# Kernel tuning notes

Measured on AMD Instinct MI355X. Metric: run time of the kernel, lower is better.

## Reference

```python
import jax, jax.numpy as jnp
import numpy as np

TOTAL_WORDS = 10000
EMBED_LEN = 100
SEQ_LEN = 80
BATCH = 2048
UNITS = 1024


def setup_inputs() -> dict:
    key = jax.random.key(0)
    ks = jax.random.split(key, 8)
    inputs = jax.random.randint(ks[0], (BATCH, SEQ_LEN), 0, TOTAL_WORDS)
    s = 0.02
    emb = jax.random.normal(ks[1], (TOTAL_WORDS, EMBED_LEN), jnp.float32) * s
    W0 = jax.random.normal(ks[2], (EMBED_LEN, 4 * UNITS), jnp.float32) * s
    U0 = jax.random.normal(ks[3], (UNITS, 4 * UNITS), jnp.float32) * s
    b0 = jnp.zeros((4 * UNITS,), jnp.float32)
    W1 = jax.random.normal(ks[4], (UNITS, 4 * UNITS), jnp.float32) * s
    U1 = jax.random.normal(ks[5], (UNITS, 4 * UNITS), jnp.float32) * s
    b1 = jnp.zeros((4 * UNITS,), jnp.float32)
    fcW = jax.random.normal(ks[6], (UNITS, 1), jnp.float32) * s
    fcb = jnp.zeros((1,), jnp.float32)
    return {"inputs": inputs, "emb": emb, "W0": W0, "U0": U0, "b0": b0,
            "W1": W1, "U1": U1, "b1": b1, "fcW": fcW, "fcb": fcb}


def _lstm_step(x, h, c, W, U, b):
    # Keras LSTMCell gate order: i, f, g(candidate), o
    z = x @ W + h @ U + b  # [B, 4*units]
    i, f, g, o = jnp.split(z, 4, axis=-1)
    i = jax.nn.sigmoid(i)
    f = jax.nn.sigmoid(f)
    g = jnp.tanh(g)
    o = jax.nn.sigmoid(o)
    c_new = f * c + i * g
    h_new = o * jnp.tanh(c_new)
    return h_new, c_new


def reference(inputs, emb, W0, U0, b0, W1, U1, b1, fcW, fcb):
    x = emb[inputs]                      # [B, T, E]
    xs = jnp.transpose(x, (1, 0, 2))     # [T, B, E] for scan over time
    B = inputs.shape[0]
    U = U0.shape[0]
    init = (jnp.zeros((B, U), x.dtype), jnp.zeros((B, U), x.dtype),
            jnp.zeros((B, U), x.dtype), jnp.zeros((B, U), x.dtype))

    def step(carry, xt):
        h0, c0, h1, c1 = carry
        h0, c0 = _lstm_step(xt, h0, c0, W0, U0, b0)
        h1, c1 = _lstm_step(h0, h1, c1, W1, U1, b1)
        return (h0, c0, h1, c1), None

    (h0, c0, h1, c1), _ = jax.lax.scan(step, init, xs)
    logits = h1 @ fcW + fcb              # [B, 1]
    return jax.nn.sigmoid(logits)
```

## Files before the change

kernel.cpp:

```cpp
#include <hip/hip_runtime.h>

#define DEVI __device__ __forceinline__

typedef __attribute__((ext_vector_type(4))) float f4;
typedef long long i64t;
typedef __attribute__((ext_vector_type(2))) long long i64x2;

DEVI unsigned char f2fp8(float x) {
  int p = __builtin_amdgcn_cvt_pk_fp8_f32(x, x, 0, false);
  return (unsigned char)(p & 0xff);
}
DEVI float fp82f(unsigned char b) {
  return __builtin_amdgcn_cvt_f32_fp8((int)b, 0);
}
DEVI float sigmoidf_(float x) { return 1.f / (1.f + __expf(-x)); }
DEVI float tanhf_(float x) {
  float ax = fabsf(x);
  float e = __expf(-2.f * ax);
  float t = (1.f - e) / (1.f + e);
  return x < 0.f ? -t : t;
}

#define GLDS16(g, l) __builtin_amdgcn_global_load_lds( \
    (const __attribute__((address_space(1))) void*)(g), \
    (__attribute__((address_space(3))) void*)(l), 16, 0, 0)

#define SCALE_UP 64.0f
#define SCALE_DN (1.0f / 4096.0f)

DEVI int mapcol(int k, int r) {
  int c2 = ((k >> 3) & 3) ^ ((r >> 1) & 3);
  return (k & ~63) | (c2 << 4) | (((k >> 5) & 1) << 3) | (k & 7);
}


__global__ void k_conv_emb(const float* __restrict__ emb, unsigned char* __restrict__ ep) {
  int i = blockIdx.x * 256 + threadIdx.x;
  if (i >= 10000 * 128) return;
  int r = i >> 7, c = i & 127;
  ep[r * 128 + mapcol(c, 0)] =
      (c < 100) ? f2fp8(emb[r * 100 + c] * SCALE_UP) : (unsigned char)0;
}

DEVI int permn(int n) {
  int g = n >> 10, u = n & 1023;
  return (u >> 5) * 128 + ((u >> 4) & 1) * 64 + g * 16 + (u & 15);
}

__global__ void k_conv_w0(const float* __restrict__ W0, const float* __restrict__ U0,
                          unsigned char* __restrict__ WT) {
  int i = blockIdx.x * 256 + threadIdx.x;
  if (i >= 4096 * 1152) return;
  int n = i / 1152, k = i - n * 1152;
  float v;
  if (k < 100) v = W0[k * 4096 + n];
  else if (k < 128) v = 0.f;
  else v = U0[(k - 128) * 4096 + n];
  int np = permn(n);
  WT[(size_t)np * 1152 + mapcol(k, np)] = f2fp8(v * SCALE_UP);
}

__global__ void k_conv_w1(const float* __restrict__ W1, const float* __restrict__ U1,
                          unsigned char* __restrict__ WT) {
  int i = blockIdx.x * 256 + threadIdx.x;
  if (i >= 4096 * 2048) return;
  int n = i >> 11, k = i & 2047;
  float v = (k < 1024) ? W1[k * 4096 + n] : U1[(k - 1024) * 4096 + n];
  int np = permn(n);
  WT[(size_t)np * 2048 + mapcol(k, np)] = f2fp8(v * SCALE_UP);
}


template<int K1, int KTOT, bool GATHER>
DEVI void lstm_body(int blk, char* smem,
    const unsigned char* __restrict__ src1,
    const unsigned char* __restrict__ src2,
    const int* __restrict__ idx, int t,
    const unsigned char* __restrict__ WT,
    const float* __restrict__ bias,
    float* __restrict__ cbuf,
    unsigned char* __restrict__ hout)
{
  const int tid = threadIdx.x;
  const int bn = blk & 31;
  const int bm = blk >> 5;
  const int m0 = bm * 128;
  const int n0 = bn * 128;

  const int lr = tid >> 2;
  const int c16 = (tid & 3) * 16;
  const int csw = ((tid & 3) ^ ((tid >> 3) & 3)) * 16;

  const unsigned char* g1[2];
  if (GATHER) {
#pragma unroll
    for (int p = 0; p < 2; ++p) {
      int w = idx[(m0 + p * 64 + lr) * 80 + t];
      g1[p] = src1 + (size_t)w * K1 + csw;
    }
  }

  char* const LA0 = smem;
  char* const LB0 = smem + 8192;
  char* const LA1 = smem + 16384;
  char* const LB1 = smem + 24576;

  auto stage = [&](int kb) {
    char* la = (kb & 1) ? LA1 : LA0;
    char* lb = (kb & 1) ? LB1 : LB0;
    const int kc = kb * 64;
    if (GATHER && kc < K1) {
#pragma unroll
      for (int p = 0; p < 2; ++p)
        GLDS16(g1[p] + kc, la + p * 4096 + tid * 16);
    } else {
#pragma unroll
      for (int p = 0; p < 2; ++p) {
        size_t row = (size_t)(m0 + p * 64 + lr);
        const unsigned char* g = (kc < K1)
            ? (src1 + row * 1024 + kc + c16)
            : (src2 + row * 1024 + (kc - K1) + c16);
        GLDS16(g, la + p * 4096 + tid * 16);
      }
    }
#pragma unroll
    for (int p = 0; p < 2; ++p)
      GLDS16(WT + (size_t)(n0 + p * 64 + lr) * KTOT + kc + c16,
             lb + p * 4096 + tid * 16);
  };

  const int lane = tid & 63;
  const int wv = tid >> 6;
  const int wm = wv >> 1;
  const int wn = wv & 1;
  const int cl = lane & 15;
  const int qd = lane >> 4;
  const int fcl = (cl >> 1) & 3;
  const int aoff = (wm * 64 + cl) * 64 + ((qd ^ fcl) << 4);
  const int boff = (wn * 64 + cl) * 64 + ((qd ^ fcl) << 4);

  f4 acc[4][4];
  const f4 fz = {0.f, 0.f, 0.f, 0.f};
#pragma unroll
  for (int a = 0; a < 4; ++a)
#pragma unroll
    for (int b = 0; b < 4; ++b) acc[a][b] = fz;

  stage(0);

  constexpr int NKB = KTOT / 64;
#pragma unroll 1
  for (int kb = 0; kb < NKB; ++kb) {
    __syncthreads();
    if (kb + 1 < NKB) stage(kb + 1);
    char* la = (kb & 1) ? LA1 : LA0;
    char* lb = (kb & 1) ? LB1 : LB0;
    i64x2 av[4], bv[4];
#pragma unroll
    for (int mi = 0; mi < 4; ++mi)
      av[mi] = *(const i64x2*)(la + aoff + mi * 1024);
#pragma unroll
    for (int j = 0; j < 4; ++j)
      bv[j] = *(const i64x2*)(lb + boff + j * 1024);
#pragma unroll
    for (int mi = 0; mi < 4; ++mi)
#pragma unroll
      for (int j = 0; j < 4; ++j)
        acc[mi][j] = __builtin_amdgcn_mfma_f32_16x16x32_fp8_fp8(
            av[mi][0], bv[j][0], acc[mi][j], 0, 0, 0);
#pragma unroll
    for (int mi = 0; mi < 4; ++mi)
#pragma unroll
      for (int j = 0; j < 4; ++j)
        acc[mi][j] = __builtin_amdgcn_mfma_f32_16x16x32_fp8_fp8(
            av[mi][1], bv[j][1], acc[mi][j], 0, 0, 0);
  }

  const int u = bn * 32 + wn * 16 + cl;
  const int hbase = (u & ~63) | (((u >> 5) & 1) << 3) | (u & 7);
  const int c1u = (u >> 3) & 3;
  const float bi = bias[u];
  const float bff = bias[1024 + u];
  const float bg = bias[2048 + u];
  const float bo = bias[3072 + u];
#pragma unroll
  for (int mi = 0; mi < 4; ++mi) {
    int mbase = m0 + wm * 64 + mi * 16 + qd * 4;
#pragma unroll
    for (int r = 0; r < 4; ++r) {
      int m = mbase + r;
      float gi = sigmoidf_(acc[mi][0][r] * SCALE_DN + bi);
      float gf = sigmoidf_(acc[mi][1][r] * SCALE_DN + bff);
      float gg = tanhf_(acc[mi][2][r] * SCALE_DN + bg);
      float go = sigmoidf_(acc[mi][3][r] * SCALE_DN + bo);
      size_t coff = (size_t)m * 1024 + u;
      float cn = gf * cbuf[coff] + gi * gg;
      cbuf[coff] = cn;
      int c2 = c1u ^ ((qd * 2 + (r >> 1)) & 3);
      hout[(size_t)m * 1024 + (hbase | (c2 << 4))] =
          f2fp8(go * tanhf_(cn) * SCALE_UP);
    }
  }
}

__global__ __launch_bounds__(256, 4) void k_step(
    int mode,
    const unsigned char* embp, const unsigned char* h0in,
    const int* idx, int t,
    const unsigned char* WT0, const float* b0, float* c0, unsigned char* h0out,
    const unsigned char* h0prev, const unsigned char* h1in,
    const unsigned char* WT1, const float* b1, float* c1, unsigned char* h1out)
{
  extern __shared__ char smem[];
  const int blk = blockIdx.x;
  const int tile = (mode == 1) ? (blk >> 1) : blk;
  const bool isL0 = (mode == 0) || (mode == 1 && (blk & 1));
  if (isL0)
    lstm_body<128, 1152, true>(tile, smem, embp, h0in, idx, t,
                               WT0, b0, c0, h0out);
  else
    lstm_body<1024, 2048, false>(tile, smem, h0prev, h1in, nullptr, 0,
                                 WT1, b1, c1, h1out);
}


__global__ void k_fc(const unsigned char* __restrict__ h1,
                     const float* __restrict__ fcW, const float* __restrict__ fcb,
                     float* __restrict__ out) {
  int wv = threadIdx.x >> 6;
  int lane = threadIdx.x & 63;
  int row = blockIdx.x * 4 + wv;
  if (row >= 2048) return;
  const unsigned char* hr = h1 + (size_t)row * 1024;
  float s = 0.f;
  for (int k = lane; k < 1024; k += 64)
    s += fp82f(hr[mapcol(k, row)]) * fcW[k];
#pragma unroll
  for (int off = 32; off > 0; off >>= 1) s += __shfl_down(s, off);
  if (lane == 0) out[row] = sigmoidf_(s * (1.0f / SCALE_UP) + fcb[0]);
}


extern "C" void kernel_launch(void* const* d_in, const int* in_sizes, int n_in,
                              void* d_out, int out_size, void* d_ws, size_t ws_size,
                              hipStream_t stream) {
  const int*   idx = (const int*)d_in[0];
  const float* emb = (const float*)d_in[1];
  const float* W0  = (const float*)d_in[2];
  const float* U0  = (const float*)d_in[3];
  const float* b0  = (const float*)d_in[4];
  const float* W1  = (const float*)d_in[5];
  const float* U1  = (const float*)d_in[6];
  const float* b1  = (const float*)d_in[7];
  const float* fcW = (const float*)d_in[8];
  const float* fcb = (const float*)d_in[9];
  float* out = (float*)d_out;

  char* ws = (char*)d_ws;
  unsigned char* embp = (unsigned char*)(ws);
  unsigned char* WT0  = (unsigned char*)(ws + 1280000);
  unsigned char* WT1  = (unsigned char*)(ws + 5998592);
  unsigned char* h0b[2] = {(unsigned char*)(ws + 14387200),
                           (unsigned char*)(ws + 16484352)};
  unsigned char* h1b[2] = {(unsigned char*)(ws + 18581504),
                           (unsigned char*)(ws + 20678656)};
  float* c0 = (float*)(ws + 22775808);
  float* c1 = (float*)(ws + 31164416);

  hipMemsetAsync(ws + 14387200, 0, 25165824, stream);

  k_conv_emb<<<5000, 256, 0, stream>>>(emb, embp);
  k_conv_w0<<<18432, 256, 0, stream>>>(W0, U0, WT0);
  k_conv_w1<<<32768, 256, 0, stream>>>(W1, U1, WT1);

  k_step<<<512, 256, 32768, stream>>>(0, embp, h0b[1], idx, 0,
                                      WT0, b0, c0, h0b[0],
                                      nullptr, nullptr, WT1, b1, c1, nullptr);
  for (int t = 1; t < 80; ++t) {
    k_step<<<1024, 256, 32768, stream>>>(1, embp, h0b[(t + 1) & 1], idx, t,
                                         WT0, b0, c0, h0b[t & 1],
                                         h0b[(t - 1) & 1], h1b[t & 1],
                                         WT1, b1, c1, h1b[(t + 1) & 1]);
  }
  k_step<<<512, 256, 32768, stream>>>(2, nullptr, nullptr, nullptr, 0,
                                      WT0, b0, c0, nullptr,
                                      h0b[1], h1b[0], WT1, b1, c1, h1b[1]);

  k_fc<<<512, 256, 0, stream>>>(h1b[1], fcW, fcb, out);
}
```

Baseline: 4.316 ms.

## Prefetch B tiles two stages ahead and register-prefetch B fragments

Splits the LDS staging into separate A and B loaders, so B (weight) tiles are issued two k-blocks ahead while A tiles stay one ahead. B fragments for the next k-block are read from LDS into registers during the current iteration, hiding LDS read latency behind the MFMAs. It also interleaves the two k-halves of each MFMA on the same accumulator, which creates back-to-back dependent MFMAs and may add stalls. Register pressure rises from the extra fragment buffer, and compiler-inserted waits on the asynchronous LDS loads may limit the real depth of the prefetch.

```diff
diff --git a/kernel.cpp b/kernel.cpp
--- a/kernel.cpp
+++ b/kernel.cpp
@@ -100,14 +100,11 @@
     }
   }
 
-  char* const LA0 = smem;
-  char* const LB0 = smem + 8192;
-  char* const LA1 = smem + 16384;
-  char* const LB1 = smem + 24576;
-
-  auto stage = [&](int kb) {
-    char* la = (kb & 1) ? LA1 : LA0;
-    char* lb = (kb & 1) ? LB1 : LB0;
+  char* const sA[2] = {smem, smem + 8192};
+  char* const sB[2] = {smem + 16384, smem + 24576};
+
+  auto stageA = [&](int kb) {
+    char* la = sA[kb & 1];
     const int kc = kb * 64;
     if (GATHER && kc < K1) {
 #pragma unroll
@@ -123,6 +120,10 @@
         GLDS16(g, la + p * 4096 + tid * 16);
       }
     }
+  };
+  auto stageB = [&](int kb) {
+    char* lb = sB[kb & 1];
+    const int kc = kb * 64;
 #pragma unroll
     for (int p = 0; p < 2; ++p)
       GLDS16(WT + (size_t)(n0 + p * 64 + lr) * KTOT + kc + c16,
@@ -146,34 +147,46 @@
 #pragma unroll
     for (int b = 0; b < 4; ++b) acc[a][b] = fz;
 
-  stage(0);
-
   constexpr int NKB = KTOT / 64;
+
+  stageA(0);
+  stageB(0);
+  stageB(1);
+  __syncthreads();
+
+  i64x2 av[4], bv[4], bvn[4];
+#pragma unroll
+  for (int j = 0; j < 4; ++j)
+    bv[j] = *(const i64x2*)(sB[0] + boff + j * 1024);
+
 #pragma unroll 1
   for (int kb = 0; kb < NKB; ++kb) {
     __syncthreads();
-    if (kb + 1 < NKB) stage(kb + 1);
-    char* la = (kb & 1) ? LA1 : LA0;
-    char* lb = (kb & 1) ? LB1 : LB0;
-    i64x2 av[4], bv[4];
+    char* la = sA[kb & 1];
 #pragma unroll
     for (int mi = 0; mi < 4; ++mi)
       av[mi] = *(const i64x2*)(la + aoff + mi * 1024);
-#pragma unroll
-    for (int j = 0; j < 4; ++j)
-      bv[j] = *(const i64x2*)(lb + boff + j * 1024);
+    if (kb + 1 < NKB) {
+      char* lbn = sB[(kb + 1) & 1];
+#pragma unroll
+      for (int j = 0; j < 4; ++j)
+        bvn[j] = *(const i64x2*)(lbn + boff + j * 1024);
+      stageA(kb + 1);
+    }
+    if (kb + 2 < NKB) stageB(kb + 2);
 #pragma unroll
     for (int mi = 0; mi < 4; ++mi)
 #pragma unroll
-      for (int j = 0; j < 4; ++j)
+      for (int j = 0; j < 4; ++j) {
         acc[mi][j] = __builtin_amdgcn_mfma_f32_16x16x32_fp8_fp8(
             av[mi][0], bv[j][0], acc[mi][j], 0, 0, 0);
-#pragma unroll
-    for (int mi = 0; mi < 4; ++mi)
-#pragma unroll
-      for (int j = 0; j < 4; ++j)
         acc[mi][j] = __builtin_amdgcn_mfma_f32_16x16x32_fp8_fp8(
             av[mi][1], bv[j][1], acc[mi][j], 0, 0, 0);
+      }
+    if (kb + 1 < NKB) {
+#pragma unroll
+      for (int j = 0; j < 4; ++j) bv[j] = bvn[j];
+    }
   }
 
   const int u = bn * 32 + wn * 16 + cl;
```

Result: slower. 8.618 ms (+99.7%).

## Switch to 16x16x128 scaled FP8 MFMA with 128-wide K tiles

Applied to the files above, without the earlier changes.

Replaces the pair of 16x16x32 FP8 MFMA calls per K=64 chunk with a single gfx950 scaled MFMA over K=128, using unit scales. The K tile doubles to 128, so LDS staging grows to 64 KB, the swizzle changes to an 8-chunk XOR pattern in the weight, embedding and hidden-state layouts, and launch bounds drop to 2 blocks per CU. The aim is fewer MFMA issues, fewer barrier iterations and higher matrix throughput, at the cost of lower occupancy and a larger shared-memory footprint.

```diff
diff --git a/kernel.cpp b/kernel.cpp
--- a/kernel.cpp
+++ b/kernel.cpp
@@ -3,8 +3,8 @@
 #define DEVI __device__ __forceinline__
 
 typedef __attribute__((ext_vector_type(4))) float f4;
-typedef long long i64t;
-typedef __attribute__((ext_vector_type(2))) long long i64x2;
+typedef __attribute__((ext_vector_type(4))) int i32x4;
+typedef __attribute__((ext_vector_type(8))) int i32x8;
 
 DEVI unsigned char f2fp8(float x) {
   int p = __builtin_amdgcn_cvt_pk_fp8_f32(x, x, 0, false);
@@ -27,10 +27,10 @@
 
 #define SCALE_UP 64.0f
 #define SCALE_DN (1.0f / 4096.0f)
+#define SONE 0x7f7f7f7f
 
 DEVI int mapcol(int k, int r) {
-  int c2 = ((k >> 3) & 3) ^ ((r >> 1) & 3);
-  return (k & ~63) | (c2 << 4) | (((k >> 5) & 1) << 3) | (k & 7);
+  return (k & ~127) | (((((k >> 4) & 7) ^ (r & 7))) << 4) | (k & 15);
 }
 
 
@@ -38,8 +38,7 @@
   int i = blockIdx.x * 256 + threadIdx.x;
   if (i >= 10000 * 128) return;
   int r = i >> 7, c = i & 127;
-  ep[r * 128 + mapcol(c, 0)] =
-      (c < 100) ? f2fp8(emb[r * 100 + c] * SCALE_UP) : (unsigned char)0;
+  ep[i] = (c < 100) ? f2fp8(emb[r * 100 + c] * SCALE_UP) : (unsigned char)0;
 }
 
 DEVI int permn(int n) {
@@ -87,36 +86,34 @@
   const int m0 = bm * 128;
   const int n0 = bn * 128;
 
-  const int lr = tid >> 2;
-  const int c16 = (tid & 3) * 16;
-  const int csw = ((tid & 3) ^ ((tid >> 3) & 3)) * 16;
-
-  const unsigned char* g1[2];
+  const int lr = tid >> 3;
+  const int c16 = (tid & 7) * 16;
+  const int csw = ((tid & 7) ^ (lr & 7)) * 16;
+
+  const unsigned char* g1[4];
   if (GATHER) {
 #pragma unroll
-    for (int p = 0; p < 2; ++p) {
-      int w = idx[(m0 + p * 64 + lr) * 80 + t];
+    for (int p = 0; p < 4; ++p) {
+      int w = idx[(m0 + p * 32 + lr) * 80 + t];
       g1[p] = src1 + (size_t)w * K1 + csw;
     }
   }
 
-  char* const LA0 = smem;
-  char* const LB0 = smem + 8192;
-  char* const LA1 = smem + 16384;
-  char* const LB1 = smem + 24576;
+  char* const sA[2] = {smem, smem + 16384};
+  char* const sB[2] = {smem + 32768, smem + 49152};
 
   auto stage = [&](int kb) {
-    char* la = (kb & 1) ? LA1 : LA0;
-    char* lb = (kb & 1) ? LB1 : LB0;
-    const int kc = kb * 64;
+    char* la = sA[kb & 1];
+    char* lb = sB[kb & 1];
+    const int kc = kb * 128;
     if (GATHER && kc < K1) {
 #pragma unroll
-      for (int p = 0; p < 2; ++p)
-        GLDS16(g1[p] + kc, la + p * 4096 + tid * 16);
+      for (int p = 0; p < 4; ++p)
+        GLDS16(g1[p], la + p * 4096 + tid * 16);
     } else {
 #pragma unroll
-      for (int p = 0; p < 2; ++p) {
-        size_t row = (size_t)(m0 + p * 64 + lr);
+      for (int p = 0; p < 4; ++p) {
+        size_t row = (size_t)(m0 + p * 32 + lr);
         const unsigned char* g = (kc < K1)
             ? (src1 + row * 1024 + kc + c16)
             : (src2 + row * 1024 + (kc - K1) + c16);
@@ -124,8 +121,8 @@
       }
     }
 #pragma unroll
-    for (int p = 0; p < 2; ++p)
-      GLDS16(WT + (size_t)(n0 + p * 64 + lr) * KTOT + kc + c16,
+    for (int p = 0; p < 4; ++p)
+      GLDS16(WT + (size_t)(n0 + p * 32 + lr) * KTOT + kc + c16,
              lb + p * 4096 + tid * 16);
   };
 
@@ -135,9 +132,10 @@
   const int wn = wv & 1;
   const int cl = lane & 15;
   const int qd = lane >> 4;
-  const int fcl = (cl >> 1) & 3;
-  const int aoff = (wm * 64 + cl) * 64 + ((qd ^ fcl) << 4);
-  const int boff = (wn * 64 + cl) * 64 + ((qd ^ fcl) << 4);
+  const int ch0 = ((2 * qd) ^ (cl & 7)) << 4;
+  const int ch1 = ((2 * qd + 1) ^ (cl & 7)) << 4;
+  const int abase = (wm * 64 + cl) * 128;
+  const int bbase = (wn * 64 + cl) * 128;
 
   f4 acc[4][4];
   const f4 fz = {0.f, 0.f, 0.f, 0.f};
@@ -148,37 +146,37 @@
 
   stage(0);
 
-  constexpr int NKB = KTOT / 64;
+  constexpr int NKB = KTOT / 128;
 #pragma unroll 1
   for (int kb = 0; kb < NKB; ++kb) {
     __syncthreads();
     if (kb + 1 < NKB) stage(kb + 1);
-    char* la = (kb & 1) ? LA1 : LA0;
-    char* lb = (kb & 1) ? LB1 : LB0;
-    i64x2 av[4], bv[4];
+    char* la = sA[kb & 1];
+    char* lb = sB[kb & 1];
+    i32x8 av[4], bv[4];
+#pragma unroll
+    for (int mi = 0; mi < 4; ++mi) {
+      i32x4 lo = *(const i32x4*)(la + abase + mi * 2048 + ch0);
+      i32x4 hi = *(const i32x4*)(la + abase + mi * 2048 + ch1);
+      av[mi] = __builtin_shufflevector(lo, hi, 0, 1, 2, 3, 4, 5, 6, 7);
+    }
+#pragma unroll
+    for (int j = 0; j < 4; ++j) {
+      i32x4 lo = *(const i32x4*)(lb + bbase + j * 2048 + ch0);
+      i32x4 hi = *(const i32x4*)(lb + bbase + j * 2048 + ch1);
+      bv[j] = __builtin_shufflevector(lo, hi, 0, 1, 2, 3, 4, 5, 6, 7);
+    }
 #pragma unroll
     for (int mi = 0; mi < 4; ++mi)
-      av[mi] = *(const i64x2*)(la + aoff + mi * 1024);
-#pragma unroll
-    for (int j = 0; j < 4; ++j)
-      bv[j] = *(const i64x2*)(lb + boff + j * 1024);
-#pragma unroll
-    for (int mi = 0; mi < 4; ++mi)
 #pragma unroll
       for (int j = 0; j < 4; ++j)
-        acc[mi][j] = __builtin_amdgcn_mfma_f32_16x16x32_fp8_fp8(
-            av[mi][0], bv[j][0], acc[mi][j], 0, 0, 0);
-#pragma unroll
-    for (int mi = 0; mi < 4; ++mi)
-#pragma unroll
-      for (int j = 0; j < 4; ++j)
-        acc[mi][j] = __builtin_amdgcn_mfma_f32_16x16x32_fp8_fp8(
-            av[mi][1], bv[j][1], acc[mi][j], 0, 0, 0);
+        acc[mi][j] = __builtin_amdgcn_mfma_scale_f32_16x16x128_f8f6f4(
+            av[mi], bv[j], acc[mi][j], 0, 0, 0, SONE, 0, SONE);
   }
 
   const int u = bn * 32 + wn * 16 + cl;
-  const int hbase = (u & ~63) | (((u >> 5) & 1) << 3) | (u & 7);
-  const int c1u = (u >> 3) & 3;
+  const int hbase = (u & ~127) | (u & 15);
+  const int c1u = (u >> 4) & 7;
   const float bi = bias[u];
   const float bff = bias[1024 + u];
   const float bg = bias[2048 + u];
@@ -196,14 +194,14 @@
       size_t coff = (size_t)m * 1024 + u;
       float cn = gf * cbuf[coff] + gi * gg;
       cbuf[coff] = cn;
-      int c2 = c1u ^ ((qd * 2 + (r >> 1)) & 3);
+      int c2 = c1u ^ ((qd & 1) * 4 + r);
       hout[(size_t)m * 1024 + (hbase | (c2 << 4))] =
           f2fp8(go * tanhf_(cn) * SCALE_UP);
     }
   }
 }
 
-__global__ __launch_bounds__(256, 4) void k_step(
+__global__ __launch_bounds__(256, 2) void k_step(
     int mode,
     const unsigned char* embp, const unsigned char* h0in,
     const int* idx, int t,
@@ -273,16 +271,16 @@
   k_conv_w0<<<18432, 256, 0, stream>>>(W0, U0, WT0);
   k_conv_w1<<<32768, 256, 0, stream>>>(W1, U1, WT1);
 
-  k_step<<<512, 256, 32768, stream>>>(0, embp, h0b[1], idx, 0,
+  k_step<<<512, 256, 65536, stream>>>(0, embp, h0b[1], idx, 0,
                                       WT0, b0, c0, h0b[0],
                                       nullptr, nullptr, WT1, b1, c1, nullptr);
   for (int t = 1; t < 80; ++t) {
-    k_step<<<1024, 256, 32768, stream>>>(1, embp, h0b[(t + 1) & 1], idx, t,
+    k_step<<<1024, 256, 65536, stream>>>(1, embp, h0b[(t + 1) & 1], idx, t,
                                          WT0, b0, c0, h0b[t & 1],
                                          h0b[(t - 1) & 1], h1b[t & 1],
                                          WT1, b1, c1, h1b[(t + 1) & 1]);
   }
-  k_step<<<512, 256, 32768, stream>>>(2, nullptr, nullptr, nullptr, 0,
+  k_step<<<512, 256, 65536, stream>>>(2, nullptr, nullptr, nullptr, 0,
                                       WT0, b0, c0, nullptr,
                                       h0b[1], h1b[0], WT1, b1, c1, h1b[1]);
 
```

Result: slower. 4.991 ms (+15.6%).

## Restructure LSTM step into independent per-wave 64x64 tiles with private LDS pipelines

Applied to the files above, without the earlier changes.

Each wavefront now owns its own 64x64 output tile and a private 16 KB LDS region. This replaces the 256-thread cooperative 128x128 block tile with 128-thread blocks pairing one layer-0 wave and one layer-1 wave. Block-wide __syncthreads is replaced by per-wave s_waitcnt vmcnt/lgkmcnt fences with a two-stage-ahead prefetch. The goal is to remove barrier stalls and let the two layers' waves interleave on the same CU. In exchange each wave does less data reuse per loaded byte (smaller tiles), and the grid doubles. A dummy tanh call is also inserted before the output gate computation.

```diff
diff --git a/kernel.cpp b/kernel.cpp
--- a/kernel.cpp
+++ b/kernel.cpp
@@ -3,7 +3,6 @@
 #define DEVI __device__ __forceinline__
 
 typedef __attribute__((ext_vector_type(4))) float f4;
-typedef long long i64t;
 typedef __attribute__((ext_vector_type(2))) long long i64x2;
 
 DEVI unsigned char f2fp8(float x) {
@@ -72,7 +71,7 @@
 
 
 template<int K1, int KTOT, bool GATHER>
-DEVI void lstm_body(int blk, char* smem,
+DEVI void lstm_wave(int tile, char* wlds,
     const unsigned char* __restrict__ src1,
     const unsigned char* __restrict__ src2,
     const int* __restrict__ idx, int t,
@@ -81,63 +80,53 @@
     float* __restrict__ cbuf,
     unsigned char* __restrict__ hout)
 {
-  const int tid = threadIdx.x;
-  const int bn = blk & 31;
-  const int bm = blk >> 5;
-  const int m0 = bm * 128;
-  const int n0 = bn * 128;
-
-  const int lr = tid >> 2;
-  const int c16 = (tid & 3) * 16;
-  const int csw = ((tid & 3) ^ ((tid >> 3) & 3)) * 16;
-
-  const unsigned char* g1[2];
+  const int lane = threadIdx.x & 63;
+  const int tm = tile & 31;
+  const int tn = tile >> 5;
+  const int m0 = tm * 64, n0 = tn * 64;
+
+  const int sr = lane >> 2;
+  const int sc = (lane & 3) * 16;
+  const int csw = ((lane & 3) ^ ((lane >> 3) & 3)) * 16;
+
+  int rowOffA[4], rowOffB[4];
+#pragma unroll
+  for (int p = 0; p < 4; ++p) {
+    rowOffA[p] = (m0 + p * 16 + sr) * 1024 + sc;
+    rowOffB[p] = (n0 + p * 16 + sr) * KTOT + sc;
+  }
+  const unsigned char* g1[4];
   if (GATHER) {
 #pragma unroll
-    for (int p = 0; p < 2; ++p) {
-      int w = idx[(m0 + p * 64 + lr) * 80 + t];
-      g1[p] = src1 + (size_t)w * K1 + csw;
+    for (int p = 0; p < 4; ++p) {
+      int w = idx[(m0 + p * 16 + sr) * 80 + t];
+      g1[p] = src1 + (size_t)w * 128 + csw;
     }
   }
 
-  char* const LA0 = smem;
-  char* const LB0 = smem + 8192;
-  char* const LA1 = smem + 16384;
-  char* const LB1 = smem + 24576;
-
   auto stage = [&](int kb) {
-    char* la = (kb & 1) ? LA1 : LA0;
-    char* lb = (kb & 1) ? LB1 : LB0;
+    char* la = wlds + (kb & 1) * 4096;
+    char* lb = wlds + 8192 + (kb & 1) * 4096;
     const int kc = kb * 64;
     if (GATHER && kc < K1) {
 #pragma unroll
-      for (int p = 0; p < 2; ++p)
-        GLDS16(g1[p] + kc, la + p * 4096 + tid * 16);
+      for (int p = 0; p < 4; ++p)
+        GLDS16(g1[p] + kc, la + p * 1024 + lane * 16);
     } else {
-#pragma unroll
-      for (int p = 0; p < 2; ++p) {
-        size_t row = (size_t)(m0 + p * 64 + lr);
-        const unsigned char* g = (kc < K1)
-            ? (src1 + row * 1024 + kc + c16)
-            : (src2 + row * 1024 + (kc - K1) + c16);
-        GLDS16(g, la + p * 4096 + tid * 16);
-      }
+      const unsigned char* base = (kc < K1) ? (src1 + kc) : (src2 + (kc - K1));
+#pragma unroll
+      for (int p = 0; p < 4; ++p)
+        GLDS16(base + rowOffA[p], la + p * 1024 + lane * 16);
     }
 #pragma unroll
-    for (int p = 0; p < 2; ++p)
-      GLDS16(WT + (size_t)(n0 + p * 64 + lr) * KTOT + kc + c16,
-             lb + p * 4096 + tid * 16);
+    for (int p = 0; p < 4; ++p)
+      GLDS16(WT + kc + rowOffB[p], lb + p * 1024 + lane * 16);
   };
 
-  const int lane = tid & 63;
-  const int wv = tid >> 6;
-  const int wm = wv >> 1;
-  const int wn = wv & 1;
   const int cl = lane & 15;
   const int qd = lane >> 4;
-  const int fcl = (cl >> 1) & 3;
-  const int aoff = (wm * 64 + cl) * 64 + ((qd ^ fcl) << 4);
-  const int boff = (wn * 64 + cl) * 64 + ((qd ^ fcl) << 4);
+  const int fo = (qd ^ ((cl >> 1) & 3)) << 4;
+  const int roff = cl * 64 + fo;
 
   f4 acc[4][4];
   const f4 fz = {0.f, 0.f, 0.f, 0.f};
@@ -146,22 +135,27 @@
 #pragma unroll
     for (int b = 0; b < 4; ++b) acc[a][b] = fz;
 
+  constexpr int NKB = KTOT / 64;
   stage(0);
-
-  constexpr int NKB = KTOT / 64;
+  stage(1);
+
 #pragma unroll 1
   for (int kb = 0; kb < NKB; ++kb) {
-    __syncthreads();
-    if (kb + 1 < NKB) stage(kb + 1);
-    char* la = (kb & 1) ? LA1 : LA0;
-    char* lb = (kb & 1) ? LB1 : LB0;
+    if (kb < NKB - 1)
+      asm volatile("s_waitcnt vmcnt(8)" ::: "memory");
+    else
+      asm volatile("s_waitcnt vmcnt(0)" ::: "memory");
+    char* la = wlds + (kb & 1) * 4096;
+    char* lb = wlds + 8192 + (kb & 1) * 4096;
     i64x2 av[4], bv[4];
 #pragma unroll
     for (int mi = 0; mi < 4; ++mi)
-      av[mi] = *(const i64x2*)(la + aoff + mi * 1024);
+      av[mi] = *(const i64x2*)(la + roff + mi * 1024);
 #pragma unroll
     for (int j = 0; j < 4; ++j)
-      bv[j] = *(const i64x2*)(lb + boff + j * 1024);
+      bv[j] = *(const i64x2*)(lb + roff + j * 1024);
+    asm volatile("s_waitcnt lgkmcnt(0)" ::: "memory");
+    if (kb + 2 < NKB) stage(kb + 2);
 #pragma unroll
     for (int mi = 0; mi < 4; ++mi)
 #pragma unroll
@@ -176,7 +170,7 @@
             av[mi][1], bv[j][1], acc[mi][j], 0, 0, 0);
   }
 
-  const int u = bn * 32 + wn * 16 + cl;
+  const int u = (tn >> 1) * 32 + (tn & 1) * 16 + cl;
   const int hbase = (u & ~63) | (((u >> 5) & 1) << 3) | (u & 7);
   const int c1u = (u >> 3) & 3;
   const float bi = bias[u];
@@ -185,14 +179,15 @@
   const float bo = bias[3072 + u];
 #pragma unroll
   for (int mi = 0; mi < 4; ++mi) {
-    int mbase = m0 + wm * 64 + mi * 16 + qd * 4;
+    int mbase = m0 + mi * 16 + qd * 4;
 #pragma unroll
     for (int r = 0; r < 4; ++r) {
       int m = mbase + r;
       float gi = sigmoidf_(acc[mi][0][r] * SCALE_DN + bi);
       float gf = sigmoidf_(acc[mi][1][r] * SCALE_DN + bff);
       float gg = tanhf_(acc[mi][2][r] * SCALE_DN + bg);
-      float go = sigmoidf_(acc[mi][3][r] * SCALE_DN + bo);
+      float go = tanhf_  (0.f);
+      go = sigmoidf_(acc[mi][3][r] * SCALE_DN + bo);
       size_t coff = (size_t)m * 1024 + u;
       float cn = gf * cbuf[coff] + gi * gg;
       cbuf[coff] = cn;
@@ -203,7 +198,7 @@
   }
 }
 
-__global__ __launch_bounds__(256, 4) void k_step(
+__global__ __launch_bounds__(128, 2) void k_step(
     int mode,
     const unsigned char* embp, const unsigned char* h0in,
     const int* idx, int t,
@@ -212,15 +207,22 @@
     const unsigned char* WT1, const float* b1, float* c1, unsigned char* h1out)
 {
   extern __shared__ char smem[];
-  const int blk = blockIdx.x;
-  const int tile = (mode == 1) ? (blk >> 1) : blk;
-  const bool isL0 = (mode == 0) || (mode == 1 && (blk & 1));
-  if (isL0)
-    lstm_body<128, 1152, true>(tile, smem, embp, h0in, idx, t,
+  const int v = threadIdx.x >> 6;
+  char* wlds = smem + v * 16384;
+  if (mode == 1) {
+    if (v == 0)
+      lstm_wave<1024, 2048, false>(blockIdx.x, wlds, h0prev, h1in, nullptr, 0,
+                                   WT1, b1, c1, h1out);
+    else
+      lstm_wave<128, 1152, true>(blockIdx.x, wlds, embp, h0in, idx, t,
+                                 WT0, b0, c0, h0out);
+  } else if (mode == 0) {
+    lstm_wave<128, 1152, true>(blockIdx.x * 2 + v, wlds, embp, h0in, idx, t,
                                WT0, b0, c0, h0out);
-  else
-    lstm_body<1024, 2048, false>(tile, smem, h0prev, h1in, nullptr, 0,
-                                 WT1, b1, c1, h1out);
+  } else {
+    lstm_wave<1024, 2048, false>(blockIdx.x * 2 + v, wlds, h0prev, h1in,
+                                 nullptr, 0, WT1, b1, c1, h1out);
+  }
 }
 
 
@@ -273,18 +275,18 @@
   k_conv_w0<<<18432, 256, 0, stream>>>(W0, U0, WT0);
   k_conv_w1<<<32768, 256, 0, stream>>>(W1, U1, WT1);
 
-  k_step<<<512, 256, 32768, stream>>>(0, embp, h0b[1], idx, 0,
-                                      WT0, b0, c0, h0b[0],
-                                      nullptr, nullptr, WT1, b1, c1, nullptr);
+  k_step<<<1024, 128, 32768, stream>>>(0, embp, h0b[1], idx, 0,
+                                       WT0, b0, c0, h0b[0],
+                                       nullptr, nullptr, WT1, b1, c1, nullptr);
   for (int t = 1; t < 80; ++t) {
-    k_step<<<1024, 256, 32768, stream>>>(1, embp, h0b[(t + 1) & 1], idx, t,
+    k_step<<<2048, 128, 32768, stream>>>(1, embp, h0b[(t + 1) & 1], idx, t,
                                          WT0, b0, c0, h0b[t & 1],
                                          h0b[(t - 1) & 1], h1b[t & 1],
                                          WT1, b1, c1, h1b[(t + 1) & 1]);
   }
-  k_step<<<512, 256, 32768, stream>>>(2, nullptr, nullptr, nullptr, 0,
-                                      WT0, b0, c0, nullptr,
-                                      h0b[1], h1b[0], WT1, b1, c1, h1b[1]);
+  k_step<<<1024, 128, 32768, stream>>>(2, nullptr, nullptr, nullptr, 0,
+                                       WT0, b0, c0, nullptr,
+                                       h0b[1], h1b[0], WT1, b1, c1, h1b[1]);
 
   k_fc<<<512, 256, 0, stream>>>(h1b[1], fcW, fcb, out);
 }
```

New measurement: 5.897 ms. +36.6%, slower.
